# Kernel tuning notes

Measured on AMD Instinct MI355X. Metric: run time of the kernel, lower is better.

Reference implementation:

```python
import jax, jax.numpy as jnp
import numpy as np

H, D, IN, E, N = 4, 16, 64, 400000, 100000
RELS = [("c1c1", "C1", "C1"), ("c1c2", "C1", "C2"), ("c1c3", "C1", "C3"),
        ("c2c1", "C2", "C1"), ("c2c2", "C2", "C2"), ("c2c3", "C2", "C3"),
        ("c3c1", "C3", "C1"), ("c3c2", "C3", "C2"), ("c3c3", "C3", "C3")]
TYPES = ("C1", "C2", "C3")


def setup_inputs() -> dict:
    key = jax.random.key(0)
    ks = iter(jax.random.split(key, 128))
    inp = {}
    for t in TYPES:
        inp["feat_" + t] = jax.random.normal(next(ks), (N, IN), jnp.float32)
        inp["W_" + t] = jax.random.normal(next(ks), (IN, H * D), jnp.float32) * 0.05
        inp["b_" + t] = jnp.zeros((H * D,), jnp.float32)
    for r, s, d in RELS:
        inp["W_" + r] = jax.random.normal(next(ks), (IN, H * D), jnp.float32) * 0.05
        inp["b_" + r] = jnp.zeros((H * D,), jnp.float32)
        inp["asrc_" + r] = jax.random.normal(next(ks), (H, D), jnp.float32) * 0.1
        inp["adst_" + r] = jax.random.normal(next(ks), (H, D), jnp.float32) * 0.1
        inp["src_" + r] = jax.random.randint(next(ks), (E,), 0, N, jnp.int32)
        inp["dst_" + r] = jax.random.randint(next(ks), (E,), 0, N, jnp.int32)
    return inp


def _forward(feats, selfp, relp):
    # leaky_relu with negative_slope = l_alpha = 0.2
    lrelu = lambda x: jnp.where(x >= 0, x, 0.2 * x)
    # per-type self projections Wh_T  [N, H, D]
    Wh_self = {t: (feats[t] @ selfp[t][0] + selfp[t][1]).reshape(-1, H, D) for t in TYPES}
    agg = {t: jnp.zeros((feats[t].shape[0], H, D), feats[t].dtype) for t in TYPES}
    for r, s, d in RELS:
        W, b, asrc, adst, src, dst = relp[r]
        # project once per source node, then gather per edge (same math as per-edge fc)
        Wh = (feats[s] @ W + b).reshape(-1, H, D)      # [Ns, H, D]
        whe = Wh[src]                                   # [E, H, D]
        # attention logits: (Wh_e * a_src).sum(-1) + (Wh_self_dst * a_dst).sum(-1)
        e = lrelu((whe * asrc).sum(-1) + (Wh_self[d][dst] * adst).sum(-1))  # [E, H]
        # nn.Softmax(dim=1) in the original acts over the heads axis of [E, H, 1]
        alpha = jax.nn.softmax(e, axis=1)[..., None]    # [E, H, 1]
        agg[d] = agg[d] + jax.ops.segment_sum(whe * alpha, dst, num_segments=agg[d].shape[0])
    return tuple(jax.nn.relu(agg[t]) for t in TYPES)


def reference(feat_C1, feat_C2, feat_C3, W_C1, b_C1, W_C2, b_C2, W_C3, b_C3,
              W_c1c1, b_c1c1, asrc_c1c1, adst_c1c1, src_c1c1, dst_c1c1,
              W_c1c2, b_c1c2, asrc_c1c2, adst_c1c2, src_c1c2, dst_c1c2,
              W_c1c3, b_c1c3, asrc_c1c3, adst_c1c3, src_c1c3, dst_c1c3,
              W_c2c1, b_c2c1, asrc_c2c1, adst_c2c1, src_c2c1, dst_c2c1,
              W_c2c2, b_c2c2, asrc_c2c2, adst_c2c2, src_c2c2, dst_c2c2,
              W_c2c3, b_c2c3, asrc_c2c3, adst_c2c3, src_c2c3, dst_c2c3,
              W_c3c1, b_c3c1, asrc_c3c1, adst_c3c1, src_c3c1, dst_c3c1,
              W_c3c2, b_c3c2, asrc_c3c2, adst_c3c2, src_c3c2, dst_c3c2,
              W_c3c3, b_c3c3, asrc_c3c3, adst_c3c3, src_c3c3, dst_c3c3):
    L = dict(locals())
    feats = {t: L["feat_" + t] for t in TYPES}
    selfp = {t: (L["W_" + t], L["b_" + t]) for t in TYPES}
    relp = {r: (L["W_" + r], L["b_" + r], L["asrc_" + r], L["adst_" + r], L["src_" + r], L["dst_" + r]) for r, _, _ in RELS}
    return _forward(feats, selfp, relp)
```

## Files before the change

kernel.cpp:

```cpp
#include <hip/hip_runtime.h>
#include <hip/hip_bf16.h>

constexpr int IN_F = 64;
constexpr int HD   = 64;
constexpr int BN   = 128;

constexpr int BW_BITS = 10;
constexpr int BWIDTH  = 1 << BW_BITS;
constexpr int BCAP    = 6144;
constexpr int BIN_EPT = 16;
constexpr int BIN_CHUNK = 256 * BIN_EPT;

static __device__ __forceinline__ float bf2f(unsigned short u) {
  union { unsigned int i; float f; } c; c.i = ((unsigned int)u) << 16; return c.f;
}

struct ProjParams {
  const float* feat[3];
  const float* Wp[3][4];
  const float* bp[3][4];
  const float* adst[9];
  const float* asrc[9];
  __hip_bfloat16* wh[9];
  float* sdot[9];
  float* ddot[9];
  int N;
};

__global__ __launch_bounds__(256) void proj_kernel(ProjParams p) {
  const int t  = blockIdx.y;
  const int n0 = blockIdx.x * BN;
  const int tid = threadIdx.x;
  const int N = p.N;

  __shared__ float featL[BN][IN_F + 1];
  __shared__ float WL[IN_F][HD];

  {
    const float* feat = p.feat[t];
    for (int i = tid; i < BN * (IN_F / 4); i += 256) {
      const int row = i >> 4;
      const int c4  = (i & 15) << 2;
      float4 v = make_float4(0.f, 0.f, 0.f, 0.f);
      const int n = n0 + row;
      if (n < N) v = *(const float4*)(feat + (size_t)n * IN_F + c4);
      featL[row][c4 + 0] = v.x; featL[row][c4 + 1] = v.y;
      featL[row][c4 + 2] = v.z; featL[row][c4 + 3] = v.w;
    }
  }

  const int node = tid >> 2;
  const int cg   = tid & 3;
  const int cg16 = cg * 16;
  const int nA   = n0 + node;
  const int nB   = n0 + node + 64;

  for (int pr = 0; pr < 4; ++pr) {
    __syncthreads();
    {
      const float* W = p.Wp[t][pr];
      for (int i = tid; i < IN_F * HD / 4; i += 256) {
        *(float4*)(&WL[0][0] + i * 4) = *(const float4*)(W + i * 4);
      }
    }
    __syncthreads();

    const float* b = p.bp[t][pr];
    float acc0[16], acc1[16];
    #pragma unroll
    for (int jj = 0; jj < 16; ++jj) { acc0[jj] = b[cg16 + jj]; acc1[jj] = acc0[jj]; }

    #pragma unroll 4
    for (int k = 0; k < IN_F; ++k) {
      const float a0 = featL[node][k];
      const float a1 = featL[node + 64][k];
      const float4 w0 = *(const float4*)(&WL[k][cg16 + 0]);
      const float4 w1 = *(const float4*)(&WL[k][cg16 + 4]);
      const float4 w2 = *(const float4*)(&WL[k][cg16 + 8]);
      const float4 w3 = *(const float4*)(&WL[k][cg16 + 12]);
      acc0[0]  = fmaf(a0, w0.x, acc0[0]);  acc0[1]  = fmaf(a0, w0.y, acc0[1]);
      acc0[2]  = fmaf(a0, w0.z, acc0[2]);  acc0[3]  = fmaf(a0, w0.w, acc0[3]);
      acc0[4]  = fmaf(a0, w1.x, acc0[4]);  acc0[5]  = fmaf(a0, w1.y, acc0[5]);
      acc0[6]  = fmaf(a0, w1.z, acc0[6]);  acc0[7]  = fmaf(a0, w1.w, acc0[7]);
      acc0[8]  = fmaf(a0, w2.x, acc0[8]);  acc0[9]  = fmaf(a0, w2.y, acc0[9]);
      acc0[10] = fmaf(a0, w2.z, acc0[10]); acc0[11] = fmaf(a0, w2.w, acc0[11]);
      acc0[12] = fmaf(a0, w3.x, acc0[12]); acc0[13] = fmaf(a0, w3.y, acc0[13]);
      acc0[14] = fmaf(a0, w3.z, acc0[14]); acc0[15] = fmaf(a0, w3.w, acc0[15]);
      acc1[0]  = fmaf(a1, w0.x, acc1[0]);  acc1[1]  = fmaf(a1, w0.y, acc1[1]);
      acc1[2]  = fmaf(a1, w0.z, acc1[2]);  acc1[3]  = fmaf(a1, w0.w, acc1[3]);
      acc1[4]  = fmaf(a1, w1.x, acc1[4]);  acc1[5]  = fmaf(a1, w1.y, acc1[5]);
      acc1[6]  = fmaf(a1, w1.z, acc1[6]);  acc1[7]  = fmaf(a1, w1.w, acc1[7]);
      acc1[8]  = fmaf(a1, w2.x, acc1[8]);  acc1[9]  = fmaf(a1, w2.y, acc1[9]);
      acc1[10] = fmaf(a1, w2.z, acc1[10]); acc1[11] = fmaf(a1, w2.w, acc1[11]);
      acc1[12] = fmaf(a1, w3.x, acc1[12]); acc1[13] = fmaf(a1, w3.y, acc1[13]);
      acc1[14] = fmaf(a1, w3.z, acc1[14]); acc1[15] = fmaf(a1, w3.w, acc1[15]);
    }

    if (pr == 0) {
      #pragma unroll
      for (int sj = 0; sj < 3; ++sj) {
        const int ri = sj * 3 + t;
        const float* ad = p.adst[ri] + cg16;
        float s0 = 0.f, s1 = 0.f;
        #pragma unroll
        for (int jj = 0; jj < 16; ++jj) {
          const float av = ad[jj];
          s0 = fmaf(acc0[jj], av, s0);
          s1 = fmaf(acc1[jj], av, s1);
        }
        if (nA < N) p.ddot[ri][(size_t)nA * 4 + cg] = s0;
        if (nB < N) p.ddot[ri][(size_t)nB * 4 + cg] = s1;
      }
    } else {
      const int ri = t * 3 + (pr - 1);
      const float* as = p.asrc[ri] + cg16;
      float s0 = 0.f, s1 = 0.f;
      #pragma unroll
      for (int jj = 0; jj < 16; ++jj) {
        const float av = as[jj];
        s0 = fmaf(acc0[jj], av, s0);
        s1 = fmaf(acc1[jj], av, s1);
      }
      if (nA < N) {
        __hip_bfloat16* whp = p.wh[ri] + (size_t)nA * HD + cg16;
        #pragma unroll
        for (int jj = 0; jj < 16; ++jj) whp[jj] = __float2bfloat16(acc0[jj]);
        p.sdot[ri][(size_t)nA * 4 + cg] = s0;
      }
      if (nB < N) {
        __hip_bfloat16* whp = p.wh[ri] + (size_t)nB * HD + cg16;
        #pragma unroll
        for (int jj = 0; jj < 16; ++jj) whp[jj] = __float2bfloat16(acc1[jj]);
        p.sdot[ri][(size_t)nB * 4 + cg] = s1;
      }
    }
  }
}

struct EdgeLists { const int* src[9]; const int* dst[9]; int E; int N; };

__global__ __launch_bounds__(256) void zero_u32_kernel(unsigned* p, int n) {
  const int i = blockIdx.x * 256 + threadIdx.x;
  if (i < n) p[i] = 0u;
}

__global__ __launch_bounds__(256) void bin_kernel(EdgeLists el, unsigned* bcnt,
                                                  unsigned* binBuf, int nbuck) {
  const int r   = blockIdx.y;
  const int tid = threadIdx.x;
  const int e0  = blockIdx.x * BIN_CHUNK;
  const int E   = el.E;
  const int* srcp = el.src[r];
  const int* dstp = el.dst[r];

  __shared__ unsigned bh[128], bcur[128], bbase[128];
  if (tid < 128) { bh[tid] = 0u; bcur[tid] = 0u; }
  __syncthreads();

  int sv[BIN_EPT], dv[BIN_EPT];
  #pragma unroll
  for (int i = 0; i < BIN_EPT; ++i) {
    const int e = e0 + i * 256 + tid;
    if (e < E) {
      sv[i] = srcp[e];
      dv[i] = dstp[e];
      atomicAdd(&bh[dv[i] >> BW_BITS], 1u);
    } else dv[i] = -1;
  }
  __syncthreads();

  if (tid < 128) {
    bbase[tid] = (tid < nbuck && bh[tid] > 0u)
                   ? atomicAdd(bcnt + (size_t)r * nbuck + tid, bh[tid]) : 0u;
  }
  __syncthreads();

  unsigned* bb = binBuf + (size_t)r * nbuck * BCAP;
  #pragma unroll
  for (int i = 0; i < BIN_EPT; ++i) {
    if (dv[i] >= 0) {
      const int b = dv[i] >> BW_BITS;
      const unsigned pos = bbase[b] + atomicAdd(&bcur[b], 1u);
      if (pos < (unsigned)BCAP)
        bb[(size_t)b * BCAP + pos] = (unsigned)sv[i] | ((unsigned)(dv[i] & (BWIDTH - 1)) << 17);
    }
  }
}

__global__ __launch_bounds__(64) void bscan_kernel(unsigned* bcnt, unsigned* bscan, int nbuck) {
  const int r = blockIdx.x;
  if (threadIdx.x == 0) {
    unsigned run = 0;
    for (int b = 0; b < nbuck; ++b) {
      unsigned c = bcnt[(size_t)r * nbuck + b];
      if (c > (unsigned)BCAP) c = BCAP;
      bcnt[(size_t)r * nbuck + b] = c;
      bscan[(size_t)r * nbuck + b] = run;
      run += c;
    }
  }
}

__global__ __launch_bounds__(256) void csr_kernel(const unsigned* binBuf,
                                                  const unsigned* bcnt,
                                                  const unsigned* bscan,
                                                  unsigned* offsets,
                                                  unsigned* perm,
                                                  int N, int E, int nbuck) {
  const int r   = blockIdx.y;
  const int b   = blockIdx.x;
  const int tid = threadIdx.x;
  const unsigned cnt  = bcnt[(size_t)r * nbuck + b];
  const unsigned base = bscan[(size_t)r * nbuck + b];
  const unsigned* buf = binBuf + ((size_t)r * nbuck + b) * BCAP;
  unsigned* offr = offsets + (size_t)r * (N + 1);
  unsigned* permr = perm + (size_t)r * E;

  __shared__ unsigned S[BWIDTH];
  __shared__ unsigned T[256];
  __shared__ unsigned permL[BCAP];

  for (int i = tid; i < BWIDTH; i += 256) S[i] = 0u;
  __syncthreads();

  for (unsigned i = tid; i < cnt; i += 256) atomicAdd(&S[buf[i] >> 17], 1u);
  __syncthreads();

  const int b4 = tid * 4;
  unsigned loc0 = S[b4], loc1 = S[b4 + 1], loc2 = S[b4 + 2], loc3 = S[b4 + 3];
  unsigned s = loc0 + loc1 + loc2 + loc3;
  T[tid] = s;
  __syncthreads();
  for (int d = 1; d < 256; d <<= 1) {
    const unsigned v = T[tid];
    const unsigned a = (tid >= d) ? T[tid - d] : 0u;
    __syncthreads();
    T[tid] = v + a;
    __syncthreads();
  }
  unsigned run = T[tid] - s;
  S[b4]     = run;  run += loc0;
  S[b4 + 1] = run;  run += loc1;
  S[b4 + 2] = run;  run += loc2;
  S[b4 + 3] = run;
  __syncthreads();

  const int d0 = b * BWIDTH;
  for (int i = tid; i < BWIDTH; i += 256) {
    const int d = d0 + i;
    if (d < N) offr[d] = base + S[i];
  }
  if (b == 0 && tid == 0) offr[N] = (unsigned)E;
  __syncthreads();

  for (unsigned i = tid; i < cnt; i += 256) {
    const unsigned v = buf[i];
    const unsigned pos = atomicAdd(&S[v >> 17], 1u);
    permL[pos] = v & 0x1FFFFu;
  }
  __syncthreads();

  for (unsigned i = tid; i < cnt; i += 256) permr[base + i] = permL[i];
}

struct AggParams {
  const unsigned* offsets[9];
  const unsigned* perm[9];
  const float* sdot[9];
  const float* ddot[9];
  const unsigned short* wh[9];
  float* outp[3];
  int N, E;
};

typedef __attribute__((ext_vector_type(4))) unsigned short us4;

__global__ __launch_bounds__(256) void agg_kernel(AggParams p) {
  const int t    = blockIdx.y;
  const int w    = threadIdx.x >> 6;
  const int lane = threadIdx.x & 63;
  const int n    = blockIdx.x * 4 + w;
  if (n >= p.N) return;
  const int slot = lane >> 4;
  const int l16  = lane & 15;
  const int h    = l16 >> 2;

  float acc0 = 0.f, acc1 = 0.f, acc2 = 0.f, acc3 = 0.f;

  #pragma unroll
  for (int sj = 0; sj < 3; ++sj) {
    const int r = sj * 3 + t;
    const unsigned start = p.offsets[r][n];
    const unsigned end   = p.offsets[r][n + 1];
    if (start == end) continue;
    const float4 dd = *(const float4*)(p.ddot[r] + (size_t)n * 4);
    const unsigned* pm = p.perm[r];
    const float* sdr = p.sdot[r];
    const unsigned short* whr = p.wh[r];

    for (unsigned base = start; base < end; base += 4) {
      const unsigned pos  = base + slot;
      const unsigned posc = (pos < end) ? pos : (end - 1);
      const unsigned s = pm[posc];
      const float4 sd = *(const float4*)(sdr + (size_t)s * 4);
      float e0 = sd.x + dd.x, e1 = sd.y + dd.y, e2 = sd.z + dd.z, e3 = sd.w + dd.w;
      e0 = (e0 >= 0.f) ? e0 : 0.2f * e0;
      e1 = (e1 >= 0.f) ? e1 : 0.2f * e1;
      e2 = (e2 >= 0.f) ? e2 : 0.2f * e2;
      e3 = (e3 >= 0.f) ? e3 : 0.2f * e3;
      const float m = fmaxf(fmaxf(e0, e1), fmaxf(e2, e3));
      const float x0 = __expf(e0 - m);
      const float x1 = __expf(e1 - m);
      const float x2 = __expf(e2 - m);
      const float x3 = __expf(e3 - m);
      const float inv = 1.f / (x0 + x1 + x2 + x3);
      float a = ((h == 0) ? x0 : (h == 1) ? x1 : (h == 2) ? x2 : x3) * inv;
      if (pos >= end) a = 0.f;
      const us4 wv = *(const us4*)(whr + (size_t)s * HD + l16 * 4);
      acc0 = fmaf(a, bf2f(wv.x), acc0);
      acc1 = fmaf(a, bf2f(wv.y), acc1);
      acc2 = fmaf(a, bf2f(wv.z), acc2);
      acc3 = fmaf(a, bf2f(wv.w), acc3);
    }
  }

  acc0 += __shfl_xor(acc0, 16); acc1 += __shfl_xor(acc1, 16);
  acc2 += __shfl_xor(acc2, 16); acc3 += __shfl_xor(acc3, 16);
  acc0 += __shfl_xor(acc0, 32); acc1 += __shfl_xor(acc1, 32);
  acc2 += __shfl_xor(acc2, 32); acc3 += __shfl_xor(acc3, 32);

  if (slot == 0) {
    float4 v;
    v.x = fmaxf(acc0, 0.f); v.y = fmaxf(acc1, 0.f);
    v.z = fmaxf(acc2, 0.f); v.w = fmaxf(acc3, 0.f);
    *(float4*)(p.outp[t] + (size_t)n * HD + l16 * 4) = v;
  }
}

extern "C" void kernel_launch(void* const* d_in, const int* in_sizes, int n_in,
                              void* d_out, int out_size, void* d_ws, size_t ws_size,
                              hipStream_t stream) {
  const int N = in_sizes[0] / IN_F;
  const int E = in_sizes[9 + 4];
  const int nbuck = (N + BWIDTH - 1) >> BW_BITS;

  ProjParams pp; AggParams ap; EdgeLists el;
  pp.N = N; ap.N = N; ap.E = E; el.E = E; el.N = N;

  for (int t = 0; t < 3; ++t) {
    pp.feat[t]  = (const float*)d_in[t * 3 + 0];
    pp.Wp[t][0] = (const float*)d_in[t * 3 + 1];
    pp.bp[t][0] = (const float*)d_in[t * 3 + 2];
    for (int j = 0; j < 3; ++j) {
      const int base = 9 + (t * 3 + j) * 6;
      pp.Wp[t][1 + j] = (const float*)d_in[base + 0];
      pp.bp[t][1 + j] = (const float*)d_in[base + 1];
    }
  }

  char* ws = (char*)d_ws;
  const size_t whBytes  = (size_t)N * HD * sizeof(__hip_bfloat16);
  const size_t dotBytes = (size_t)N * 4 * sizeof(float);
  char* whBase   = ws;
  char* sdotBase = whBase + 9 * whBytes;
  char* ddotBase = sdotBase + 9 * dotBytes;
  unsigned* offsets = (unsigned*)(ddotBase + 9 * dotBytes);
  unsigned* bcnt    = offsets + (size_t)9 * (N + 1);
  unsigned* bscan   = bcnt + (size_t)9 * ((nbuck + 63) & ~63);
  unsigned* perm    = bscan + (size_t)9 * ((nbuck + 63) & ~63);
  unsigned* binBuf  = perm + (size_t)9 * E;

  for (int ri = 0; ri < 9; ++ri) {
    const int base = 9 + ri * 6;
    pp.asrc[ri] = (const float*)d_in[base + 2];
    pp.adst[ri] = (const float*)d_in[base + 3];
    pp.wh[ri]   = (__hip_bfloat16*)(whBase + (size_t)ri * whBytes);
    pp.sdot[ri] = (float*)(sdotBase + (size_t)ri * dotBytes);
    pp.ddot[ri] = (float*)(ddotBase + (size_t)ri * dotBytes);
    el.src[ri]  = (const int*)d_in[base + 4];
    el.dst[ri]  = (const int*)d_in[base + 5];
    ap.wh[ri]   = (const unsigned short*)pp.wh[ri];
    ap.sdot[ri] = pp.sdot[ri];
    ap.ddot[ri] = pp.ddot[ri];
    ap.offsets[ri] = offsets + (size_t)ri * (N + 1);
    ap.perm[ri]    = perm + (size_t)ri * E;
  }
  for (int t = 0; t < 3; ++t) ap.outp[t] = (float*)d_out + (size_t)t * N * HD;

  const int nbc = 9 * nbuck;
  zero_u32_kernel<<<dim3((nbc + 255) / 256), 256, 0, stream>>>(bcnt, nbc);
  bin_kernel<<<dim3((E + BIN_CHUNK - 1) / BIN_CHUNK, 9), 256, 0, stream>>>(el, bcnt, binBuf, nbuck);
  bscan_kernel<<<dim3(9), 64, 0, stream>>>(bcnt, bscan, nbuck);
  csr_kernel<<<dim3(nbuck, 9), 256, 0, stream>>>(binBuf, bcnt, bscan, offsets, perm, N, E, nbuck);

  proj_kernel<<<dim3((N + BN - 1) / BN, 3), 256, 0, stream>>>(pp);

  agg_kernel<<<dim3((N + 3) / 4, 3), 256, 0, stream>>>(ap);
}
```

Before: 656.7 us.

## Precompute per-edge softmax weights in CSR kernel, store bf16 alphas

Moves the attention-logit, leaky-relu and head-softmax computation out of the aggregation kernel into the CSR build kernel, which now runs after the projection. Each edge's four softmax weights are stored as packed bf16 in CSR order. The aggregation kernel then reads a single bf16 weight per lane instead of gathering sdot/ddot and recomputing exp. This removes redundant softmax work, which was repeated by all 16 lanes sharing an edge, and the random sdot gathers from agg. In exchange it adds a 9*E*8-byte write and read, and the attention weights are rounded to bf16.

```diff
diff --git a/kernel.cpp b/kernel.cpp
--- a/kernel.cpp
+++ b/kernel.cpp
@@ -13,6 +13,9 @@
 
 static __device__ __forceinline__ float bf2f(unsigned short u) {
   union { unsigned int i; float f; } c; c.i = ((unsigned int)u) << 16; return c.f;
+}
+static __device__ __forceinline__ unsigned short f2bf_bits(float f) {
+  union { __hip_bfloat16 h; unsigned short u; } c; c.h = __float2bfloat16(f); return c.u;
 }
 
 struct ProjParams {
@@ -201,20 +204,31 @@
   }
 }
 
-__global__ __launch_bounds__(256) void csr_kernel(const unsigned* binBuf,
-                                                  const unsigned* bcnt,
-                                                  const unsigned* bscan,
-                                                  unsigned* offsets,
-                                                  unsigned* perm,
-                                                  int N, int E, int nbuck) {
+struct CsrParams {
+  const unsigned* binBuf;
+  const unsigned* bcnt;
+  const unsigned* bscan;
+  unsigned* offsets;
+  unsigned* perm;
+  unsigned short* alf;
+  const float* sdot[9];
+  const float* ddot[9];
+  int N, E, nbuck;
+};
+
+__global__ __launch_bounds__(256) void csr_kernel(CsrParams cp) {
   const int r   = blockIdx.y;
   const int b   = blockIdx.x;
   const int tid = threadIdx.x;
-  const unsigned cnt  = bcnt[(size_t)r * nbuck + b];
-  const unsigned base = bscan[(size_t)r * nbuck + b];
-  const unsigned* buf = binBuf + ((size_t)r * nbuck + b) * BCAP;
-  unsigned* offr = offsets + (size_t)r * (N + 1);
-  unsigned* permr = perm + (size_t)r * E;
+  const int N = cp.N, E = cp.E, nbuck = cp.nbuck;
+  const unsigned cnt  = cp.bcnt[(size_t)r * nbuck + b];
+  const unsigned base = cp.bscan[(size_t)r * nbuck + b];
+  const unsigned* buf = cp.binBuf + ((size_t)r * nbuck + b) * BCAP;
+  unsigned* offr = cp.offsets + (size_t)r * (N + 1);
+  unsigned* permr = cp.perm + (size_t)r * E;
+  unsigned short* alfr = cp.alf + (size_t)r * E * 4;
+  const float* sdr = cp.sdot[r];
+  const float* ddr = cp.ddot[r];
 
   __shared__ unsigned S[BWIDTH];
   __shared__ unsigned T[256];
@@ -256,18 +270,40 @@
   for (unsigned i = tid; i < cnt; i += 256) {
     const unsigned v = buf[i];
     const unsigned pos = atomicAdd(&S[v >> 17], 1u);
-    permL[pos] = v & 0x1FFFFu;
-  }
-  __syncthreads();
-
-  for (unsigned i = tid; i < cnt; i += 256) permr[base + i] = permL[i];
+    permL[pos] = v;
+  }
+  __syncthreads();
+
+  for (unsigned i = tid; i < cnt; i += 256) {
+    const unsigned v = permL[i];
+    const unsigned sv = v & 0x1FFFFu;
+    const int dn = d0 + (int)(v >> 17);
+    permr[base + i] = sv;
+
+    const float4 sd = *(const float4*)(sdr + (size_t)sv * 4);
+    const float4 dd = *(const float4*)(ddr + (size_t)dn * 4);
+    float e0 = sd.x + dd.x, e1 = sd.y + dd.y, e2 = sd.z + dd.z, e3 = sd.w + dd.w;
+    e0 = (e0 >= 0.f) ? e0 : 0.2f * e0;
+    e1 = (e1 >= 0.f) ? e1 : 0.2f * e1;
+    e2 = (e2 >= 0.f) ? e2 : 0.2f * e2;
+    e3 = (e3 >= 0.f) ? e3 : 0.2f * e3;
+    const float m = fmaxf(fmaxf(e0, e1), fmaxf(e2, e3));
+    const float x0 = __expf(e0 - m);
+    const float x1 = __expf(e1 - m);
+    const float x2 = __expf(e2 - m);
+    const float x3 = __expf(e3 - m);
+    const float inv = 1.f / (x0 + x1 + x2 + x3);
+    uint2 packed;
+    packed.x = ((unsigned)f2bf_bits(x1 * inv) << 16) | f2bf_bits(x0 * inv);
+    packed.y = ((unsigned)f2bf_bits(x3 * inv) << 16) | f2bf_bits(x2 * inv);
+    *(uint2*)(alfr + (size_t)(base + i) * 4) = packed;
+  }
 }
 
 struct AggParams {
   const unsigned* offsets[9];
   const unsigned* perm[9];
-  const float* sdot[9];
-  const float* ddot[9];
+  const unsigned short* alf[9];
   const unsigned short* wh[9];
   float* outp[3];
   int N, E;
@@ -292,29 +328,15 @@
     const int r = sj * 3 + t;
     const unsigned start = p.offsets[r][n];
     const unsigned end   = p.offsets[r][n + 1];
-    if (start == end) continue;
-    const float4 dd = *(const float4*)(p.ddot[r] + (size_t)n * 4);
     const unsigned* pm = p.perm[r];
-    const float* sdr = p.sdot[r];
+    const unsigned short* al = p.alf[r];
     const unsigned short* whr = p.wh[r];
 
     for (unsigned base = start; base < end; base += 4) {
       const unsigned pos  = base + slot;
       const unsigned posc = (pos < end) ? pos : (end - 1);
       const unsigned s = pm[posc];
-      const float4 sd = *(const float4*)(sdr + (size_t)s * 4);
-      float e0 = sd.x + dd.x, e1 = sd.y + dd.y, e2 = sd.z + dd.z, e3 = sd.w + dd.w;
-      e0 = (e0 >= 0.f) ? e0 : 0.2f * e0;
-      e1 = (e1 >= 0.f) ? e1 : 0.2f * e1;
-      e2 = (e2 >= 0.f) ? e2 : 0.2f * e2;
-      e3 = (e3 >= 0.f) ? e3 : 0.2f * e3;
-      const float m = fmaxf(fmaxf(e0, e1), fmaxf(e2, e3));
-      const float x0 = __expf(e0 - m);
-      const float x1 = __expf(e1 - m);
-      const float x2 = __expf(e2 - m);
-      const float x3 = __expf(e3 - m);
-      const float inv = 1.f / (x0 + x1 + x2 + x3);
-      float a = ((h == 0) ? x0 : (h == 1) ? x1 : (h == 2) ? x2 : x3) * inv;
+      float a = bf2f(al[posc * 4 + h]);
       if (pos >= end) a = 0.f;
       const us4 wv = *(const us4*)(whr + (size_t)s * HD + l16 * 4);
       acc0 = fmaf(a, bf2f(wv.x), acc0);
@@ -344,8 +366,9 @@
   const int E = in_sizes[9 + 4];
   const int nbuck = (N + BWIDTH - 1) >> BW_BITS;
 
-  ProjParams pp; AggParams ap; EdgeLists el;
+  ProjParams pp; AggParams ap; EdgeLists el; CsrParams cp;
   pp.N = N; ap.N = N; ap.E = E; el.E = E; el.N = N;
+  cp.N = N; cp.E = E; cp.nbuck = nbuck;
 
   for (int t = 0; t < 3; ++t) {
     pp.feat[t]  = (const float*)d_in[t * 3 + 0];
@@ -368,7 +391,11 @@
   unsigned* bcnt    = offsets + (size_t)9 * (N + 1);
   unsigned* bscan   = bcnt + (size_t)9 * ((nbuck + 63) & ~63);
   unsigned* perm    = bscan + (size_t)9 * ((nbuck + 63) & ~63);
-  unsigned* binBuf  = perm + (size_t)9 * E;
+  unsigned short* alf = (unsigned short*)(perm + (size_t)9 * E);
+  unsigned* binBuf  = (unsigned*)(alf + (size_t)9 * E * 4);
+
+  cp.offsets = offsets; cp.perm = perm; cp.alf = alf;
+  cp.binBuf = binBuf; cp.bcnt = bcnt; cp.bscan = bscan;
 
   for (int ri = 0; ri < 9; ++ri) {
     const int base = 9 + ri * 6;
@@ -379,9 +406,10 @@
     pp.ddot[ri] = (float*)(ddotBase + (size_t)ri * dotBytes);
     el.src[ri]  = (const int*)d_in[base + 4];
     el.dst[ri]  = (const int*)d_in[base + 5];
+    cp.sdot[ri] = pp.sdot[ri];
+    cp.ddot[ri] = pp.ddot[ri];
     ap.wh[ri]   = (const unsigned short*)pp.wh[ri];
-    ap.sdot[ri] = pp.sdot[ri];
-    ap.ddot[ri] = pp.ddot[ri];
+    ap.alf[ri]  = alf + (size_t)ri * E * 4;
     ap.offsets[ri] = offsets + (size_t)ri * (N + 1);
     ap.perm[ri]    = perm + (size_t)ri * E;
   }
@@ -391,9 +419,10 @@
   zero_u32_kernel<<<dim3((nbc + 255) / 256), 256, 0, stream>>>(bcnt, nbc);
   bin_kernel<<<dim3((E + BIN_CHUNK - 1) / BIN_CHUNK, 9), 256, 0, stream>>>(el, bcnt, binBuf, nbuck);
   bscan_kernel<<<dim3(9), 64, 0, stream>>>(bcnt, bscan, nbuck);
-  csr_kernel<<<dim3(nbuck, 9), 256, 0, stream>>>(binBuf, bcnt, bscan, offsets, perm, N, E, nbuck);
 
   proj_kernel<<<dim3((N + BN - 1) / BN, 3), 256, 0, stream>>>(pp);
 
+  csr_kernel<<<dim3(nbuck, 9), 256, 0, stream>>>(cp);
+
   agg_kernel<<<dim3((N + 3) / 4, 3), 256, 0, stream>>>(ap);
 }
```

New measurement: 689.3 us. 5.0% more time.
